# Kernel optimization log

Hardware: AMD Instinct MI355X
Metric: run time of the kernel (lower is better)

Reference implementation:

```python
import jax, jax.numpy as jnp
import numpy as np

D_MODEL = 1024
D_FF = 2 * D_MODEL
N_EXPERTS = 8
TOP_K = 2
SCAT_SCALE = 0.1


def setup_inputs() -> dict:
    key = jax.random.key(0)
    ks = jax.random.split(key, 8)
    s_in = 1.0 / np.sqrt(D_MODEL)
    s_ff = 1.0 / np.sqrt(D_FF)
    return {
        "x": jax.random.normal(ks[0], (4, 2048, D_MODEL), dtype=jnp.float32),
        "Wg": jax.random.uniform(ks[1], (D_MODEL, N_EXPERTS), minval=-s_in, maxval=s_in),
        "bg": jax.random.uniform(ks[2], (N_EXPERTS,), minval=-s_in, maxval=s_in),
        "W1": jax.random.uniform(ks[3], (N_EXPERTS, D_MODEL, D_FF), minval=-s_in, maxval=s_in),
        "b1": jax.random.uniform(ks[4], (N_EXPERTS, D_FF), minval=-s_in, maxval=s_in),
        "W2": jax.random.uniform(ks[5], (N_EXPERTS, D_FF, D_MODEL), minval=-s_ff, maxval=s_ff),
        "b2": jax.random.uniform(ks[6], (N_EXPERTS, D_MODEL), minval=-s_ff, maxval=s_ff),
    }


def reference(x, Wg, bg, W1, b1, W2, b2):
    B, N, D = x.shape
    T = B * N
    xf = x.reshape(T, D)

    # gating logits + norm-based modulation (scattering_scale branch)
    logits = xf @ Wg + bg  # [T, E]
    tnorm = jnp.linalg.norm(xf, axis=-1, keepdims=True)  # [T, 1]
    norm_scaled = (tnorm - tnorm.mean()) / (jnp.std(tnorm, ddof=1) + 1e-6)
    logits = logits + SCAT_SCALE * norm_scaled

    # top-k routing
    topv, topi = jax.lax.top_k(logits, TOP_K)  # [T, K]
    gates_k = jax.nn.softmax(topv, axis=-1)  # [T, K]
    routing_entropy = -(gates_k * jnp.log(jnp.clip(gates_k, 1e-8, None))).sum(-1).mean()

    # dense per-token expert-weight matrix (zeros for non-selected experts)
    E = W1.shape[0]
    gates = jnp.zeros((T, E), dtype=gates_k.dtype).at[
        jnp.arange(T)[:, None], topi
    ].add(gates_k)  # [T, E]

    # all-expert MLP (dense equivalent of sparse dispatch; weight 0 -> no contribution)
    h = jax.nn.relu(jnp.einsum("td,edf->etf", xf, W1) + b1[:, None, :])  # [E, T, F]
    y = jnp.einsum("etf,efd->etd", h, W2) + b2[:, None, :]  # [E, T, D]
    out = jnp.einsum("etd,te->td", y, gates).reshape(B, N, D)
    return out, routing_entropy
```

## Files before the change

kernel.cpp:

```cpp
#include <hip/hip_runtime.h>
#include <hip/hip_bf16.h>

#define T_TOK 8192
#define DMODEL 1024
#define DFF 2048
#define NEXP 8

typedef __attribute__((ext_vector_type(8))) short short8v;
typedef __attribute__((ext_vector_type(4))) float floatx4;
typedef __attribute__((ext_vector_type(4))) ushort ushort4v;

__device__ __forceinline__ ushort f2bf(float f) {
  union { float f; unsigned u; } v; v.f = f;
  unsigned u = v.u;
  unsigned r = (u + 0x7FFFu + ((u >> 16) & 1u)) >> 16;
  return (ushort)r;
}
__device__ __forceinline__ float bf2f(ushort b) {
  union { unsigned u; float f; } v; v.u = ((unsigned)b) << 16;
  return v.f;
}
__device__ __forceinline__ void gload16(const void* g, void* l) {
  __builtin_amdgcn_global_load_lds(
      (const __attribute__((address_space(1))) unsigned int*)g,
      (__attribute__((address_space(3))) unsigned int*)l, 16, 0, 0);
}
__device__ __forceinline__ short8v dsr128(unsigned off) {
  short8v r;
  asm volatile("ds_read_b128 %0, %1" : "=v"(r) : "v"(off));
  return r;
}
#define VMW(n) asm volatile("s_waitcnt vmcnt(" #n ")" ::: "memory")
#define LG0()  asm volatile("s_waitcnt lgkmcnt(0)" ::: "memory")
#define BAR()  asm volatile("s_barrier" ::: "memory")
#define SB0()  __builtin_amdgcn_sched_barrier(0)

__global__ void init_kernel(int* __restrict__ meta, float* __restrict__ entWs) {
  if (threadIdx.x < 64) meta[threadIdx.x] = 0;
  if (threadIdx.x == 0) *entWs = 0.f;
}

__global__ __launch_bounds__(256) void gating_kernel(
    const float* __restrict__ x, const float* __restrict__ Wg,
    const float* __restrict__ bg, int* __restrict__ meta,
    int* __restrict__ te, float* __restrict__ tg, float* __restrict__ entWs,
    ushort* __restrict__ xb) {
  __shared__ float wgT[8448];
  __shared__ float sbg[NEXP];
  __shared__ int cnt_s[NEXP];
  __shared__ float ent_s;
  int tid = threadIdx.x;
#pragma unroll
  for (int k = 0; k < 8; ++k) {
    int g4 = tid + 256 * k;
    float4 v = ((const float4*)Wg)[g4];
    int q = g4 * 4;
    int f = q >> 5;
    wgT[q + f]     = v.x;
    wgT[q + 1 + f] = v.y;
    wgT[q + 2 + f] = v.z;
    wgT[q + 3 + f] = v.w;
  }
  if (tid < NEXP) { sbg[tid] = bg[tid]; cnt_s[tid] = 0; }
  if (tid == 0) ent_s = 0.f;
  __syncthreads();

  int wid = tid >> 6, lane = tid & 63;
#pragma unroll 1
  for (int it = 0; it < 4; ++it) {
    int t = blockIdx.x * 16 + wid * 4 + it;
    const float* xr = x + (long)t * DMODEL;
    ushort* xbr = xb + (long)t * DMODEL;
    float acc[NEXP];
#pragma unroll
    for (int e = 0; e < NEXP; ++e) acc[e] = 0.f;
#pragma unroll
    for (int i = 0; i < 4; ++i) {
      int dbase = i * 256 + lane * 4;
      int pad = i * 64 + lane;
      float4 xv = *(const float4*)(xr + dbase);
      ushort4v s;
      s[0] = f2bf(xv.x); s[1] = f2bf(xv.y); s[2] = f2bf(xv.z); s[3] = f2bf(xv.w);
      *(ushort4v*)(xbr + dbase) = s;
      float xj[4] = {xv.x, xv.y, xv.z, xv.w};
#pragma unroll
      for (int j = 0; j < 4; ++j) {
        int base = 8 * (dbase + j) + pad;
#pragma unroll
        for (int e = 0; e < NEXP; ++e) acc[e] += xj[j] * wgT[base + e];
      }
    }
#pragma unroll
    for (int off = 32; off; off >>= 1)
#pragma unroll
      for (int e = 0; e < NEXP; ++e) acc[e] += __shfl_xor(acc[e], off, 64);
    if (lane == 0) {
      float lg[NEXP];
#pragma unroll
      for (int e = 0; e < NEXP; ++e) lg[e] = acc[e] + sbg[e];
      int e1 = 0; float v1 = lg[0];
#pragma unroll
      for (int e = 1; e < NEXP; ++e) if (lg[e] > v1) { v1 = lg[e]; e1 = e; }
      int e2 = -1; float v2 = -1e30f;
#pragma unroll
      for (int e = 0; e < NEXP; ++e) if (e != e1 && lg[e] > v2) { v2 = lg[e]; e2 = e; }
      float p2 = expf(v2 - v1);
      float s = 1.f + p2;
      float g1 = 1.f / s, g2 = p2 / s;
      float ent = -(g1 * logf(fmaxf(g1, 1e-8f)) + g2 * logf(fmaxf(g2, 1e-8f)));
      atomicAdd(&cnt_s[e1], 1);
      atomicAdd(&cnt_s[e2], 1);
      atomicAdd(&ent_s, ent);
      te[2 * t] = e1; te[2 * t + 1] = e2;
      tg[2 * t] = g1; tg[2 * t + 1] = g2;
    }
  }
  __syncthreads();
  if (tid < NEXP && cnt_s[tid]) atomicAdd(&meta[tid], cnt_s[tid]);
  if (tid == 0) atomicAdd(entWs, ent_s * (1.f / T_TOK));
}

__global__ void prefix_kernel(int* __restrict__ meta) {
  if (threadIdx.x == 0) {
    int s = 0;
    for (int e = 0; e < NEXP; ++e) { meta[16 + e] = s; s += meta[e]; meta[32 + e] = 0; }
  }
}

__global__ void scatter_kernel(const int* __restrict__ te, const float* __restrict__ tg,
                               int* __restrict__ meta, int* __restrict__ tok,
                               float* __restrict__ gate, int* __restrict__ slotOf) {
  int t = blockIdx.x * blockDim.x + threadIdx.x;
  if (t >= T_TOK) return;
  for (int k = 0; k < 2; ++k) {
    int e = te[2 * t + k];
    int pos = atomicAdd(&meta[32 + e], 1);
    int slot = meta[16 + e] + pos;
    tok[slot] = t;
    gate[slot] = tg[2 * t + k];
    slotOf[2 * t + k] = slot;
  }
}

__global__ __launch_bounds__(256) void tcvt_kernel(const float* __restrict__ src,
                                                   ushort* __restrict__ dst,
                                                   int R, int C) {
  __shared__ ushort tile[64][72];
  int tid = threadIdx.x;
  long eoff = (long)blockIdx.z * R * C;
  int r0 = blockIdx.y * 64, c0 = blockIdx.x * 64;
  int lr = tid >> 4, lc = (tid & 15) * 4;
#pragma unroll
  for (int p = 0; p < 4; ++p) {
    int r = lr + p * 16;
    float4 v = *(const float4*)&src[eoff + (long)(r0 + r) * C + (c0 + lc)];
    tile[r][lc + 0] = f2bf(v.x); tile[r][lc + 1] = f2bf(v.y);
    tile[r][lc + 2] = f2bf(v.z); tile[r][lc + 3] = f2bf(v.w);
  }
  __syncthreads();
  int sr = tid >> 3, sc = (tid & 7) * 8;
#pragma unroll
  for (int p = 0; p < 2; ++p) {
    int c = sr + p * 32;
    short8v v;
#pragma unroll
    for (int j = 0; j < 8; ++j) v[j] = (short)tile[sc + j][c];
    *(short8v*)&dst[eoff + (long)(c0 + c) * R + (r0 + sc)] = v;
  }
}

__device__ __forceinline__ void gemm_pipe(
    int NT, const char* aP0, const char* aP1, const char* bP0, const char* bP1,
    char* lds, int tid, floatx4 (&acc)[8][4]) {
  const unsigned ldsU = (unsigned)(unsigned long)lds;
  int lane = tid & 63, wid = tid >> 6;
  int wm = (wid >> 2) * 128, wn = (wid & 3) * 64;
  int lr = lane & 15, lg = lane >> 4;
  unsigned offA[8], offB[4];
#pragma unroll
  for (int mi = 0; mi < 8; ++mi) {
    int row = wm + mi * 16 + lr;
    offA[mi] = row * 64 + ((lg * 16) ^ (((row >> 1) & 3) << 4));
  }
#pragma unroll
  for (int ni = 0; ni < 4; ++ni) {
    int row = wn + ni * 16 + lr;
    offB[ni] = row * 64 + ((lg * 16) ^ (((row >> 1) & 3) << 4));
  }
  int r0 = tid >> 2, r1 = r0 + 128;
  unsigned scol0 = ((tid & 3) * 16) ^ (((r0 >> 1) & 3) << 4);
  unsigned scol1 = ((tid & 3) * 16) ^ (((r1 >> 1) & 3) << 4);

  auto STG_A = [&](int buf, int ks, int t) {
    int koff = t * 128 + ks * 64;
    int reg = (buf * 2 + ks) * 16384;
    gload16(aP0 + koff + scol0, lds + reg + tid * 16);
    gload16(aP1 + koff + scol1, lds + reg + 8192 + tid * 16);
  };
  auto STG_B = [&](int buf, int ks, int t) {
    int koff = t * 128 + ks * 64;
    int reg = 65536 + (buf * 2 + ks) * 16384;
    gload16(bP0 + koff + scol0, lds + reg + tid * 16);
    gload16(bP1 + koff + scol1, lds + reg + 8192 + tid * 16);
  };
  auto RDA = [&](int buf, int ks, int mi) {
    return dsr128(ldsU + (unsigned)((buf * 2 + ks) * 16384) + offA[mi]);
  };
  auto RDB = [&](int buf, int ks, int ni) {
    return dsr128(ldsU + (unsigned)(65536 + (buf * 2 + ks) * 16384) + offB[ni]);
  };
  auto MM = [&](int mh, short8v* af, short8v* bf) {
#pragma unroll
    for (int mi = 0; mi < 4; ++mi)
#pragma unroll
      for (int ni = 0; ni < 4; ++ni)
        acc[mh * 4 + mi][ni] =
            __builtin_amdgcn_mfma_f32_16x16x32_bf16(af[mi], bf[ni], acc[mh * 4 + mi][ni], 0, 0, 0);
  };

  STG_A(0, 0, 0); STG_B(0, 0, 0);
  STG_A(0, 1, 0); STG_B(0, 1, 0);
  STG_A(1, 0, 1); STG_B(1, 0, 1);
  VMW(8); BAR();

  short8v af[4], bf0[4], bf1[4];
  for (int t = 0; t + 2 < NT; ++t) {
    int buf = t & 1, nb = buf ^ 1;
#pragma unroll
    for (int ni = 0; ni < 4; ++ni) bf0[ni] = RDB(buf, 0, ni);
#pragma unroll
    for (int i = 0; i < 4; ++i) af[i] = RDA(buf, 0, i);
    STG_A(nb, 1, t + 1);
    BAR(); LG0(); SB0();
    __builtin_amdgcn_s_setprio(1); MM(0, af, bf0); __builtin_amdgcn_s_setprio(0);
    SB0(); BAR();
#pragma unroll
    for (int i = 0; i < 4; ++i) af[i] = RDA(buf, 0, 4 + i);
    STG_B(nb, 1, t + 1);
    VMW(8);
    BAR(); LG0(); SB0();
    __builtin_amdgcn_s_setprio(1); MM(1, af, bf0); __builtin_amdgcn_s_setprio(0);
    SB0(); BAR();
#pragma unroll
    for (int ni = 0; ni < 4; ++ni) bf1[ni] = RDB(buf, 1, ni);
#pragma unroll
    for (int i = 0; i < 4; ++i) af[i] = RDA(buf, 1, i);
    STG_A(buf, 0, t + 2);
    BAR(); LG0(); SB0();
    __builtin_amdgcn_s_setprio(1); MM(0, af, bf1); __builtin_amdgcn_s_setprio(0);
    SB0(); BAR();
#pragma unroll
    for (int i = 0; i < 4; ++i) af[i] = RDA(buf, 1, 4 + i);
    STG_B(buf, 0, t + 2);
    VMW(8);
    BAR(); LG0(); SB0();
    __builtin_amdgcn_s_setprio(1); MM(1, af, bf1); __builtin_amdgcn_s_setprio(0);
    SB0(); BAR();
  }
  {
    int t = NT - 2, buf = t & 1, nb = buf ^ 1;
#pragma unroll
    for (int ni = 0; ni < 4; ++ni) bf0[ni] = RDB(buf, 0, ni);
#pragma unroll
    for (int i = 0; i < 4; ++i) af[i] = RDA(buf, 0, i);
    STG_A(nb, 1, t + 1);
    BAR(); LG0(); SB0();
    __builtin_amdgcn_s_setprio(1); MM(0, af, bf0); __builtin_amdgcn_s_setprio(0);
    SB0(); BAR();
#pragma unroll
    for (int i = 0; i < 4; ++i) af[i] = RDA(buf, 0, 4 + i);
    STG_B(nb, 1, t + 1);
    VMW(8);
    BAR(); LG0(); SB0();
    __builtin_amdgcn_s_setprio(1); MM(1, af, bf0); __builtin_amdgcn_s_setprio(0);
    SB0(); BAR();
#pragma unroll
    for (int ni = 0; ni < 4; ++ni) bf1[ni] = RDB(buf, 1, ni);
#pragma unroll
    for (int i = 0; i < 4; ++i) af[i] = RDA(buf, 1, i);
    BAR(); LG0(); SB0();
    __builtin_amdgcn_s_setprio(1); MM(0, af, bf1); __builtin_amdgcn_s_setprio(0);
    SB0(); BAR();
#pragma unroll
    for (int i = 0; i < 4; ++i) af[i] = RDA(buf, 1, 4 + i);
    VMW(4);
    BAR(); LG0(); SB0();
    __builtin_amdgcn_s_setprio(1); MM(1, af, bf1); __builtin_amdgcn_s_setprio(0);
    SB0(); BAR();
  }
  {
    int t = NT - 1, buf = t & 1;
#pragma unroll
    for (int ni = 0; ni < 4; ++ni) bf0[ni] = RDB(buf, 0, ni);
#pragma unroll
    for (int i = 0; i < 4; ++i) af[i] = RDA(buf, 0, i);
    BAR(); LG0(); SB0();
    __builtin_amdgcn_s_setprio(1); MM(0, af, bf0); __builtin_amdgcn_s_setprio(0);
    SB0(); BAR();
#pragma unroll
    for (int i = 0; i < 4; ++i) af[i] = RDA(buf, 0, 4 + i);
    VMW(0);
    BAR(); LG0(); SB0();
    __builtin_amdgcn_s_setprio(1); MM(1, af, bf0); __builtin_amdgcn_s_setprio(0);
    SB0(); BAR();
#pragma unroll
    for (int ni = 0; ni < 4; ++ni) bf1[ni] = RDB(buf, 1, ni);
#pragma unroll
    for (int i = 0; i < 4; ++i) af[i] = RDA(buf, 1, i);
    BAR(); LG0(); SB0();
    __builtin_amdgcn_s_setprio(1); MM(0, af, bf1); __builtin_amdgcn_s_setprio(0);
    SB0(); BAR();
#pragma unroll
    for (int i = 0; i < 4; ++i) af[i] = RDA(buf, 1, 4 + i);
    BAR(); LG0(); SB0();
    __builtin_amdgcn_s_setprio(1); MM(1, af, bf1); __builtin_amdgcn_s_setprio(0);
    SB0(); BAR();
  }
}

__global__ __launch_bounds__(512) void gemm1_kernel(
    const ushort* __restrict__ xb, const ushort* __restrict__ w1t,
    const float* __restrict__ b1, const int* __restrict__ meta,
    const int* __restrict__ tok, ushort* __restrict__ h) {
  int nwg = 32 * (DFF / 256) * NEXP;
  int flat = blockIdx.x;
  int wgid = (flat % 8) * (nwg / 8) + flat / 8;
  int m0 = (wgid % 32) * 256;
  int rest = wgid / 32;
  int n0 = (rest % (DFF / 256)) * 256;
  int e = rest / (DFF / 256);
  int cnt = meta[e];
  if (m0 >= cnt) return;
  int bas = meta[16 + e];
  __shared__ char lds[131072];
  int tid = threadIdx.x;

  const char* w1e = (const char*)(w1t + (long)e * DFF * DMODEL + (long)n0 * DMODEL);
  int r0 = tid >> 2;
  int ma = m0 + r0; if (ma >= cnt) ma = cnt - 1;
  int mb = m0 + r0 + 128; if (mb >= cnt) mb = cnt - 1;
  const char* aP0 = (const char*)xb + (long)tok[bas + ma] * (DMODEL * 2);
  const char* aP1 = (const char*)xb + (long)tok[bas + mb] * (DMODEL * 2);
  const char* bP0 = w1e + (long)r0 * (DMODEL * 2);
  const char* bP1 = w1e + (long)(r0 + 128) * (DMODEL * 2);

  floatx4 acc[8][4];
#pragma unroll
  for (int i = 0; i < 8; ++i)
#pragma unroll
    for (int j = 0; j < 4; ++j) acc[i][j] = (floatx4){0.f, 0.f, 0.f, 0.f};

  gemm_pipe(DMODEL / 64, aP0, aP1, bP0, bP1, lds, tid, acc);

  int lane = tid & 63, wid = tid >> 6;
  int wm = (wid >> 2) * 128, wn = (wid & 3) * 64;
  int lr = lane & 15, lg = lane >> 4;
  const float* b1e = b1 + e * DFF;
#pragma unroll
  for (int mi = 0; mi < 8; ++mi) {
#pragma unroll
    for (int r = 0; r < 4; ++r) {
      int m = m0 + wm + mi * 16 + lg * 4 + r;
      if (m >= cnt) continue;
      long hrow = (long)(bas + m) * DFF;
#pragma unroll
      for (int ni = 0; ni < 4; ++ni) {
        int f = n0 + wn + ni * 16 + lr;
        float v = acc[mi][ni][r] + b1e[f];
        h[hrow + f] = f2bf(fmaxf(v, 0.f));
      }
    }
  }
}

__global__ __launch_bounds__(512) void gemm2_kernel(
    const ushort* __restrict__ h, const ushort* __restrict__ w2t,
    const float* __restrict__ b2, const int* __restrict__ meta,
    const float* __restrict__ gate, ushort* __restrict__ y) {
  int nwg = 32 * (DMODEL / 256) * NEXP;
  int flat = blockIdx.x;
  int wgid = (flat % 8) * (nwg / 8) + flat / 8;
  int m0 = (wgid % 32) * 256;
  int rest = wgid / 32;
  int n0 = (rest % (DMODEL / 256)) * 256;
  int e = rest / (DMODEL / 256);
  int cnt = meta[e];
  if (m0 >= cnt) return;
  int bas = meta[16 + e];
  __shared__ char lds[131072];
  int tid = threadIdx.x;

  const char* w2e = (const char*)(w2t + (long)e * DMODEL * DFF + (long)n0 * DFF);
  int r0 = tid >> 2;
  int ma = m0 + r0; if (ma >= cnt) ma = cnt - 1;
  int mb = m0 + r0 + 128; if (mb >= cnt) mb = cnt - 1;
  const char* aP0 = (const char*)h + (long)(bas + ma) * (DFF * 2);
  const char* aP1 = (const char*)h + (long)(bas + mb) * (DFF * 2);
  const char* bP0 = w2e + (long)r0 * (DFF * 2);
  const char* bP1 = w2e + (long)(r0 + 128) * (DFF * 2);

  floatx4 acc[8][4];
#pragma unroll
  for (int i = 0; i < 8; ++i)
#pragma unroll
    for (int j = 0; j < 4; ++j) acc[i][j] = (floatx4){0.f, 0.f, 0.f, 0.f};

  gemm_pipe(DFF / 64, aP0, aP1, bP0, bP1, lds, tid, acc);

  int lane = tid & 63, wid = tid >> 6;
  int wm = (wid >> 2) * 128, wn = (wid & 3) * 64;
  int lr = lane & 15, lg = lane >> 4;
  const float* b2e = b2 + e * DMODEL;
#pragma unroll
  for (int mi = 0; mi < 8; ++mi) {
#pragma unroll
    for (int r = 0; r < 4; ++r) {
      int m = m0 + wm + mi * 16 + lg * 4 + r;
      if (m >= cnt) continue;
      int slot = bas + m;
      float g = gate[slot];
      ushort* yr = y + (long)slot * DMODEL;
#pragma unroll
      for (int ni = 0; ni < 4; ++ni) {
        int n = n0 + wn + ni * 16 + lr;
        float v = g * (acc[mi][ni][r] + b2e[n]);
        yr[n] = f2bf(v);
      }
    }
  }
}

__global__ __launch_bounds__(256) void combine_kernel(
    const ushort* __restrict__ y, const int* __restrict__ slotOf,
    const float* __restrict__ entWs, float* __restrict__ out) {
  int t = blockIdx.x;
  int s1 = slotOf[2 * t], s2 = slotOf[2 * t + 1];
  int d = threadIdx.x * 4;
  ushort4v a = *(const ushort4v*)&y[(long)s1 * DMODEL + d];
  ushort4v b = *(const ushort4v*)&y[(long)s2 * DMODEL + d];
  float4 r;
  r.x = bf2f(a[0]) + bf2f(b[0]);
  r.y = bf2f(a[1]) + bf2f(b[1]);
  r.z = bf2f(a[2]) + bf2f(b[2]);
  r.w = bf2f(a[3]) + bf2f(b[3]);
  *(float4*)&out[(long)t * DMODEL + d] = r;
  if (t == 0 && threadIdx.x == 0) out[(long)T_TOK * DMODEL] = *entWs;
}

extern "C" void kernel_launch(void* const* d_in, const int* in_sizes, int n_in,
                              void* d_out, int out_size, void* d_ws, size_t ws_size,
                              hipStream_t stream) {
  const float* x  = (const float*)d_in[0];
  const float* Wg = (const float*)d_in[1];
  const float* bg = (const float*)d_in[2];
  const float* W1 = (const float*)d_in[3];
  const float* b1 = (const float*)d_in[4];
  const float* W2 = (const float*)d_in[5];
  const float* b2 = (const float*)d_in[6];
  float* out = (float*)d_out;

  char* ws = (char*)d_ws;
  int*    meta   = (int*)(ws + 0);
  float*  entWs  = (float*)(ws + 256);
  int*    te     = (int*)(ws + 1024);
  float*  tg     = (float*)(ws + 66560);
  int*    tokA   = (int*)(ws + 132096);
  float*  gate   = (float*)(ws + 197632);
  int*    slotOf = (int*)(ws + 263168);
  ushort* xb     = (ushort*)(ws + 328704);
  ushort* w1t    = (ushort*)(ws + 17105920);
  ushort* w2t    = (ushort*)(ws + 50660352);
  ushort* h      = (ushort*)(ws + 84214784);
  ushort* y      = w1t;

  init_kernel<<<1, 64, 0, stream>>>(meta, entWs);
  gating_kernel<<<T_TOK / 16, 256, 0, stream>>>(x, Wg, bg, meta, te, tg, entWs, xb);
  prefix_kernel<<<1, 1, 0, stream>>>(meta);
  scatter_kernel<<<T_TOK / 256, 256, 0, stream>>>(te, tg, meta, tokA, gate, slotOf);
  tcvt_kernel<<<dim3(DFF / 64, DMODEL / 64, NEXP), 256, 0, stream>>>(W1, w1t, DMODEL, DFF);
  tcvt_kernel<<<dim3(DMODEL / 64, DFF / 64, NEXP), 256, 0, stream>>>(W2, w2t, DFF, DMODEL);
  gemm1_kernel<<<32 * (DFF / 256) * NEXP, 512, 0, stream>>>(xb, w1t, b1, meta, tokA, h);
  gemm2_kernel<<<32 * (DMODEL / 256) * NEXP, 512, 0, stream>>>(h, w2t, b2, meta, gate, y);
  combine_kernel<<<T_TOK, 256, 0, stream>>>(y, slotOf, entWs, out);
}
```

Baseline: 349.6 us.

## Shrink grouped GEMM tiles to 128x256 with 256 threads and triple-buffered LDS

Both expert GEMMs move from 256x256 tiles with 512 threads and 128KB LDS to 128x256 tiles with 256 threads, a K-step of 32, and a three-stage LDS ring of about 72KB. Each wave now covers all 128 rows and a 64-column slice. Launch bounds of (256,2) aim for two workgroups per CU and finer M granularity for the uneven per-expert token counts, which cuts padding waste in the last tile. In exchange, each workgroup reuses its weight tile over fewer rows, so total weight traffic goes up, and there are more barriers per FLOP.

```diff
diff --git a/kernel.cpp b/kernel.cpp
--- a/kernel.cpp
+++ b/kernel.cpp
@@ -170,44 +170,43 @@
 }
 
 __device__ __forceinline__ void gemm_pipe(
-    int NT, const char* aP0, const char* aP1, const char* bP0, const char* bP1,
+    int NT, const char* aP0, const char* aP1,
+    const char* bP0, const char* bP1, const char* bP2, const char* bP3,
     char* lds, int tid, floatx4 (&acc)[8][4]) {
   const unsigned ldsU = (unsigned)(unsigned long)lds;
   int lane = tid & 63, wid = tid >> 6;
-  int wm = (wid >> 2) * 128, wn = (wid & 3) * 64;
   int lr = lane & 15, lg = lane >> 4;
   unsigned offA[8], offB[4];
 #pragma unroll
   for (int mi = 0; mi < 8; ++mi) {
-    int row = wm + mi * 16 + lr;
+    int row = mi * 16 + lr;
     offA[mi] = row * 64 + ((lg * 16) ^ (((row >> 1) & 3) << 4));
   }
 #pragma unroll
   for (int ni = 0; ni < 4; ++ni) {
-    int row = wn + ni * 16 + lr;
+    int row = wid * 64 + ni * 16 + lr;
     offB[ni] = row * 64 + ((lg * 16) ^ (((row >> 1) & 3) << 4));
   }
-  int r0 = tid >> 2, r1 = r0 + 128;
-  unsigned scol0 = ((tid & 3) * 16) ^ (((r0 >> 1) & 3) << 4);
-  unsigned scol1 = ((tid & 3) * 16) ^ (((r1 >> 1) & 3) << 4);
-
-  auto STG_A = [&](int buf, int ks, int t) {
-    int koff = t * 128 + ks * 64;
-    int reg = (buf * 2 + ks) * 16384;
-    gload16(aP0 + koff + scol0, lds + reg + tid * 16);
-    gload16(aP1 + koff + scol1, lds + reg + 8192 + tid * 16);
+
+  auto STG_A = [&](int b, int t) {
+    int koff = t * 64;
+    char* d = lds + b * 8192;
+    gload16(aP0 + koff, d + tid * 16);
+    gload16(aP1 + koff, d + 4096 + tid * 16);
   };
-  auto STG_B = [&](int buf, int ks, int t) {
-    int koff = t * 128 + ks * 64;
-    int reg = 65536 + (buf * 2 + ks) * 16384;
-    gload16(bP0 + koff + scol0, lds + reg + tid * 16);
-    gload16(bP1 + koff + scol1, lds + reg + 8192 + tid * 16);
+  auto STG_B = [&](int b, int t) {
+    int koff = t * 64;
+    char* d = lds + 24576 + b * 16384;
+    gload16(bP0 + koff, d + tid * 16);
+    gload16(bP1 + koff, d + 4096 + tid * 16);
+    gload16(bP2 + koff, d + 8192 + tid * 16);
+    gload16(bP3 + koff, d + 12288 + tid * 16);
   };
-  auto RDA = [&](int buf, int ks, int mi) {
-    return dsr128(ldsU + (unsigned)((buf * 2 + ks) * 16384) + offA[mi]);
+  auto RDA = [&](int b, int mi) {
+    return dsr128(ldsU + (unsigned)(b * 8192) + offA[mi]);
   };
-  auto RDB = [&](int buf, int ks, int ni) {
-    return dsr128(ldsU + (unsigned)(65536 + (buf * 2 + ks) * 16384) + offB[ni]);
+  auto RDB = [&](int b, int ni) {
+    return dsr128(ldsU + (unsigned)(24576 + b * 16384) + offB[ni]);
   };
   auto MM = [&](int mh, short8v* af, short8v* bf) {
 #pragma unroll
@@ -218,131 +217,91 @@
             __builtin_amdgcn_mfma_f32_16x16x32_bf16(af[mi], bf[ni], acc[mh * 4 + mi][ni], 0, 0, 0);
   };
 
-  STG_A(0, 0, 0); STG_B(0, 0, 0);
-  STG_A(0, 1, 0); STG_B(0, 1, 0);
-  STG_A(1, 0, 1); STG_B(1, 0, 1);
-  VMW(8); BAR();
-
-  short8v af[4], bf0[4], bf1[4];
+  STG_A(0, 0); STG_B(0, 0);
+  STG_A(1, 1); STG_B(1, 1);
+  VMW(6); BAR();
+
+  short8v af[4], bf[4];
+  int b = 0;
   for (int t = 0; t + 2 < NT; ++t) {
-    int buf = t & 1, nb = buf ^ 1;
-#pragma unroll
-    for (int ni = 0; ni < 4; ++ni) bf0[ni] = RDB(buf, 0, ni);
-#pragma unroll
-    for (int i = 0; i < 4; ++i) af[i] = RDA(buf, 0, i);
-    STG_A(nb, 1, t + 1);
+    int bs = (b == 0) ? 2 : b - 1;
+#pragma unroll
+    for (int ni = 0; ni < 4; ++ni) bf[ni] = RDB(b, ni);
+#pragma unroll
+    for (int i = 0; i < 4; ++i) af[i] = RDA(b, i);
+    STG_A(bs, t + 2);
     BAR(); LG0(); SB0();
-    __builtin_amdgcn_s_setprio(1); MM(0, af, bf0); __builtin_amdgcn_s_setprio(0);
+    __builtin_amdgcn_s_setprio(1); MM(0, af, bf); __builtin_amdgcn_s_setprio(0);
     SB0(); BAR();
 #pragma unroll
-    for (int i = 0; i < 4; ++i) af[i] = RDA(buf, 0, 4 + i);
-    STG_B(nb, 1, t + 1);
-    VMW(8);
+    for (int i = 0; i < 4; ++i) af[i] = RDA(b, 4 + i);
+    STG_B(bs, t + 2);
+    VMW(6);
     BAR(); LG0(); SB0();
-    __builtin_amdgcn_s_setprio(1); MM(1, af, bf0); __builtin_amdgcn_s_setprio(0);
+    __builtin_amdgcn_s_setprio(1); MM(1, af, bf); __builtin_amdgcn_s_setprio(0);
     SB0(); BAR();
-#pragma unroll
-    for (int ni = 0; ni < 4; ++ni) bf1[ni] = RDB(buf, 1, ni);
-#pragma unroll
-    for (int i = 0; i < 4; ++i) af[i] = RDA(buf, 1, i);
-    STG_A(buf, 0, t + 2);
+    b = (b == 2) ? 0 : b + 1;
+  }
+  {
+#pragma unroll
+    for (int ni = 0; ni < 4; ++ni) bf[ni] = RDB(b, ni);
+#pragma unroll
+    for (int i = 0; i < 4; ++i) af[i] = RDA(b, i);
     BAR(); LG0(); SB0();
-    __builtin_amdgcn_s_setprio(1); MM(0, af, bf1); __builtin_amdgcn_s_setprio(0);
+    __builtin_amdgcn_s_setprio(1); MM(0, af, bf); __builtin_amdgcn_s_setprio(0);
     SB0(); BAR();
 #pragma unroll
-    for (int i = 0; i < 4; ++i) af[i] = RDA(buf, 1, 4 + i);
-    STG_B(buf, 0, t + 2);
-    VMW(8);
-    BAR(); LG0(); SB0();
-    __builtin_amdgcn_s_setprio(1); MM(1, af, bf1); __builtin_amdgcn_s_setprio(0);
-    SB0(); BAR();
-  }
-  {
-    int t = NT - 2, buf = t & 1, nb = buf ^ 1;
-#pragma unroll
-    for (int ni = 0; ni < 4; ++ni) bf0[ni] = RDB(buf, 0, ni);
-#pragma unroll
-    for (int i = 0; i < 4; ++i) af[i] = RDA(buf, 0, i);
-    STG_A(nb, 1, t + 1);
-    BAR(); LG0(); SB0();
-    __builtin_amdgcn_s_setprio(1); MM(0, af, bf0); __builtin_amdgcn_s_setprio(0);
-    SB0(); BAR();
-#pragma unroll
-    for (int i = 0; i < 4; ++i) af[i] = RDA(buf, 0, 4 + i);
-    STG_B(nb, 1, t + 1);
-    VMW(8);
-    BAR(); LG0(); SB0();
-    __builtin_amdgcn_s_setprio(1); MM(1, af, bf0); __builtin_amdgcn_s_setprio(0);
-    SB0(); BAR();
-#pragma unroll
-    for (int ni = 0; ni < 4; ++ni) bf1[ni] = RDB(buf, 1, ni);
-#pragma unroll
-    for (int i = 0; i < 4; ++i) af[i] = RDA(buf, 1, i);
-    BAR(); LG0(); SB0();
-    __builtin_amdgcn_s_setprio(1); MM(0, af, bf1); __builtin_amdgcn_s_setprio(0);
-    SB0(); BAR();
-#pragma unroll
-    for (int i = 0; i < 4; ++i) af[i] = RDA(buf, 1, 4 + i);
-    VMW(4);
-    BAR(); LG0(); SB0();
-    __builtin_amdgcn_s_setprio(1); MM(1, af, bf1); __builtin_amdgcn_s_setprio(0);
-    SB0(); BAR();
-  }
-  {
-    int t = NT - 1, buf = t & 1;
-#pragma unroll
-    for (int ni = 0; ni < 4; ++ni) bf0[ni] = RDB(buf, 0, ni);
-#pragma unroll
-    for (int i = 0; i < 4; ++i) af[i] = RDA(buf, 0, i);
-    BAR(); LG0(); SB0();
-    __builtin_amdgcn_s_setprio(1); MM(0, af, bf0); __builtin_amdgcn_s_setprio(0);
-    SB0(); BAR();
-#pragma unroll
-    for (int i = 0; i < 4; ++i) af[i] = RDA(buf, 0, 4 + i);
+    for (int i = 0; i < 4; ++i) af[i] = RDA(b, 4 + i);
     VMW(0);
     BAR(); LG0(); SB0();
-    __builtin_amdgcn_s_setprio(1); MM(1, af, bf0); __builtin_amdgcn_s_setprio(0);
+    __builtin_amdgcn_s_setprio(1); MM(1, af, bf); __builtin_amdgcn_s_setprio(0);
     SB0(); BAR();
-#pragma unroll
-    for (int ni = 0; ni < 4; ++ni) bf1[ni] = RDB(buf, 1, ni);
-#pragma unroll
-    for (int i = 0; i < 4; ++i) af[i] = RDA(buf, 1, i);
+    b = (b == 2) ? 0 : b + 1;
+  }
+  {
+#pragma unroll
+    for (int ni = 0; ni < 4; ++ni) bf[ni] = RDB(b, ni);
+#pragma unroll
+    for (int i = 0; i < 4; ++i) af[i] = RDA(b, i);
     BAR(); LG0(); SB0();
-    __builtin_amdgcn_s_setprio(1); MM(0, af, bf1); __builtin_amdgcn_s_setprio(0);
+    __builtin_amdgcn_s_setprio(1); MM(0, af, bf); __builtin_amdgcn_s_setprio(0);
     SB0(); BAR();
 #pragma unroll
-    for (int i = 0; i < 4; ++i) af[i] = RDA(buf, 1, 4 + i);
-    BAR(); LG0(); SB0();
-    __builtin_amdgcn_s_setprio(1); MM(1, af, bf1); __builtin_amdgcn_s_setprio(0);
-    SB0(); BAR();
-  }
-}
-
-__global__ __launch_bounds__(512) void gemm1_kernel(
+    for (int i = 0; i < 4; ++i) af[i] = RDA(b, 4 + i);
+    LG0(); SB0();
+    __builtin_amdgcn_s_setprio(1); MM(1, af, bf); __builtin_amdgcn_s_setprio(0);
+  }
+}
+
+__global__ __launch_bounds__(256, 2) void gemm1_kernel(
     const ushort* __restrict__ xb, const ushort* __restrict__ w1t,
     const float* __restrict__ b1, const int* __restrict__ meta,
     const int* __restrict__ tok, ushort* __restrict__ h) {
-  int nwg = 32 * (DFF / 256) * NEXP;
+  const int NWG = 64 * 8 * NEXP;
   int flat = blockIdx.x;
-  int wgid = (flat % 8) * (nwg / 8) + flat / 8;
-  int m0 = (wgid % 32) * 256;
-  int rest = wgid / 32;
-  int n0 = (rest % (DFF / 256)) * 256;
-  int e = rest / (DFF / 256);
+  int wgid = (flat % 8) * (NWG / 8) + flat / 8;
+  int m0 = (wgid & 63) * 128;
+  int rest = wgid >> 6;
+  int n0 = (rest & 7) * 256;
+  int e = rest >> 3;
   int cnt = meta[e];
   if (m0 >= cnt) return;
   int bas = meta[16 + e];
-  __shared__ char lds[131072];
+  __shared__ char lds[73728];
   int tid = threadIdx.x;
 
-  const char* w1e = (const char*)(w1t + (long)e * DFF * DMODEL + (long)n0 * DMODEL);
-  int r0 = tid >> 2;
-  int ma = m0 + r0; if (ma >= cnt) ma = cnt - 1;
-  int mb = m0 + r0 + 128; if (mb >= cnt) mb = cnt - 1;
-  const char* aP0 = (const char*)xb + (long)tok[bas + ma] * (DMODEL * 2);
-  const char* aP1 = (const char*)xb + (long)tok[bas + mb] * (DMODEL * 2);
-  const char* bP0 = w1e + (long)r0 * (DMODEL * 2);
-  const char* bP1 = w1e + (long)(r0 + 128) * (DMODEL * 2);
+  const char* w1e = (const char*)(w1t + (long)e * DFF * DMODEL);
+  int rA = tid >> 2;
+  int ch = tid & 3;
+  auto sc = [&](int row) { return (unsigned)((ch * 16) ^ (((row >> 1) & 3) << 4)); };
+  int ma0 = m0 + rA;        if (ma0 >= cnt) ma0 = cnt - 1;
+  int ma1 = m0 + rA + 64;   if (ma1 >= cnt) ma1 = cnt - 1;
+  const char* aP0 = (const char*)xb + (long)tok[bas + ma0] * (DMODEL * 2) + sc(rA);
+  const char* aP1 = (const char*)xb + (long)tok[bas + ma1] * (DMODEL * 2) + sc(rA + 64);
+  const char* bP0 = w1e + (long)(n0 + rA) * (DMODEL * 2) + sc(rA);
+  const char* bP1 = w1e + (long)(n0 + rA + 64) * (DMODEL * 2) + sc(rA + 64);
+  const char* bP2 = w1e + (long)(n0 + rA + 128) * (DMODEL * 2) + sc(rA + 128);
+  const char* bP3 = w1e + (long)(n0 + rA + 192) * (DMODEL * 2) + sc(rA + 192);
 
   floatx4 acc[8][4];
 #pragma unroll
@@ -350,22 +309,21 @@
 #pragma unroll
     for (int j = 0; j < 4; ++j) acc[i][j] = (floatx4){0.f, 0.f, 0.f, 0.f};
 
-  gemm_pipe(DMODEL / 64, aP0, aP1, bP0, bP1, lds, tid, acc);
+  gemm_pipe(DMODEL / 32, aP0, aP1, bP0, bP1, bP2, bP3, lds, tid, acc);
 
   int lane = tid & 63, wid = tid >> 6;
-  int wm = (wid >> 2) * 128, wn = (wid & 3) * 64;
   int lr = lane & 15, lg = lane >> 4;
   const float* b1e = b1 + e * DFF;
 #pragma unroll
   for (int mi = 0; mi < 8; ++mi) {
 #pragma unroll
     for (int r = 0; r < 4; ++r) {
-      int m = m0 + wm + mi * 16 + lg * 4 + r;
+      int m = m0 + mi * 16 + lg * 4 + r;
       if (m >= cnt) continue;
       long hrow = (long)(bas + m) * DFF;
 #pragma unroll
       for (int ni = 0; ni < 4; ++ni) {
-        int f = n0 + wn + ni * 16 + lr;
+        int f = n0 + wid * 64 + ni * 16 + lr;
         float v = acc[mi][ni][r] + b1e[f];
         h[hrow + f] = f2bf(fmaxf(v, 0.f));
       }
@@ -373,31 +331,35 @@
   }
 }
 
-__global__ __launch_bounds__(512) void gemm2_kernel(
+__global__ __launch_bounds__(256, 2) void gemm2_kernel(
     const ushort* __restrict__ h, const ushort* __restrict__ w2t,
     const float* __restrict__ b2, const int* __restrict__ meta,
     const float* __restrict__ gate, ushort* __restrict__ y) {
-  int nwg = 32 * (DMODEL / 256) * NEXP;
+  const int NWG = 64 * 4 * NEXP;
   int flat = blockIdx.x;
-  int wgid = (flat % 8) * (nwg / 8) + flat / 8;
-  int m0 = (wgid % 32) * 256;
-  int rest = wgid / 32;
-  int n0 = (rest % (DMODEL / 256)) * 256;
-  int e = rest / (DMODEL / 256);
+  int wgid = (flat % 8) * (NWG / 8) + flat / 8;
+  int m0 = (wgid & 63) * 128;
+  int rest = wgid >> 6;
+  int n0 = (rest & 3) * 256;
+  int e = rest >> 2;
   int cnt = meta[e];
   if (m0 >= cnt) return;
   int bas = meta[16 + e];
-  __shared__ char lds[131072];
+  __shared__ char lds[73728];
   int tid = threadIdx.x;
 
-  const char* w2e = (const char*)(w2t + (long)e * DMODEL * DFF + (long)n0 * DFF);
-  int r0 = tid >> 2;
-  int ma = m0 + r0; if (ma >= cnt) ma = cnt - 1;
-  int mb = m0 + r0 + 128; if (mb >= cnt) mb = cnt - 1;
-  const char* aP0 = (const char*)h + (long)(bas + ma) * (DFF * 2);
-  const char* aP1 = (const char*)h + (long)(bas + mb) * (DFF * 2);
-  const char* bP0 = w2e + (long)r0 * (DFF * 2);
-  const char* bP1 = w2e + (long)(r0 + 128) * (DFF * 2);
+  const char* w2e = (const char*)(w2t + (long)e * DMODEL * DFF);
+  int rA = tid >> 2;
+  int ch = tid & 3;
+  auto sc = [&](int row) { return (unsigned)((ch * 16) ^ (((row >> 1) & 3) << 4)); };
+  int ma0 = m0 + rA;        if (ma0 >= cnt) ma0 = cnt - 1;
+  int ma1 = m0 + rA + 64;   if (ma1 >= cnt) ma1 = cnt - 1;
+  const char* aP0 = (const char*)h + (long)(bas + ma0) * (DFF * 2) + sc(rA);
+  const char* aP1 = (const char*)h + (long)(bas + ma1) * (DFF * 2) + sc(rA + 64);
+  const char* bP0 = w2e + (long)(n0 + rA) * (DFF * 2) + sc(rA);
+  const char* bP1 = w2e + (long)(n0 + rA + 64) * (DFF * 2) + sc(rA + 64);
+  const char* bP2 = w2e + (long)(n0 + rA + 128) * (DFF * 2) + sc(rA + 128);
+  const char* bP3 = w2e + (long)(n0 + rA + 192) * (DFF * 2) + sc(rA + 192);
 
   floatx4 acc[8][4];
 #pragma unroll
@@ -405,24 +367,23 @@
 #pragma unroll
     for (int j = 0; j < 4; ++j) acc[i][j] = (floatx4){0.f, 0.f, 0.f, 0.f};
 
-  gemm_pipe(DFF / 64, aP0, aP1, bP0, bP1, lds, tid, acc);
+  gemm_pipe(DFF / 32, aP0, aP1, bP0, bP1, bP2, bP3, lds, tid, acc);
 
   int lane = tid & 63, wid = tid >> 6;
-  int wm = (wid >> 2) * 128, wn = (wid & 3) * 64;
   int lr = lane & 15, lg = lane >> 4;
   const float* b2e = b2 + e * DMODEL;
 #pragma unroll
   for (int mi = 0; mi < 8; ++mi) {
 #pragma unroll
     for (int r = 0; r < 4; ++r) {
-      int m = m0 + wm + mi * 16 + lg * 4 + r;
+      int m = m0 + mi * 16 + lg * 4 + r;
       if (m >= cnt) continue;
       int slot = bas + m;
       float g = gate[slot];
       ushort* yr = y + (long)slot * DMODEL;
 #pragma unroll
       for (int ni = 0; ni < 4; ++ni) {
-        int n = n0 + wn + ni * 16 + lr;
+        int n = n0 + wid * 64 + ni * 16 + lr;
         float v = g * (acc[mi][ni][r] + b2e[n]);
         yr[n] = f2bf(v);
       }
@@ -479,7 +440,7 @@
   scatter_kernel<<<T_TOK / 256, 256, 0, stream>>>(te, tg, meta, tokA, gate, slotOf);
   tcvt_kernel<<<dim3(DFF / 64, DMODEL / 64, NEXP), 256, 0, stream>>>(W1, w1t, DMODEL, DFF);
   tcvt_kernel<<<dim3(DMODEL / 64, DFF / 64, NEXP), 256, 0, stream>>>(W2, w2t, DFF, DMODEL);
-  gemm1_kernel<<<32 * (DFF / 256) * NEXP, 512, 0, stream>>>(xb, w1t, b1, meta, tokA, h);
-  gemm2_kernel<<<32 * (DMODEL / 256) * NEXP, 512, 0, stream>>>(h, w2t, b2, meta, gate, y);
+  gemm1_kernel<<<64 * 8 * NEXP, 256, 0, stream>>>(xb, w1t, b1, meta, tokA, h);
+  gemm2_kernel<<<64 * 4 * NEXP, 256, 0, stream>>>(h, w2t, b2, meta, gate, y);
   combine_kernel<<<T_TOK, 256, 0, stream>>>(y, slotOf, entWs, out);
 }
```

Result: faster. 336.7 us (-3.7%).
